# Performance work log

Measured on AMD Instinct MI355X. Metric: run time of the kernel, lower is better.

The kernel has to match this reference:

```python
import jax, jax.numpy as jnp
import numpy as np

E = 8      # number of experts (sublayers)
N = 8192   # tokens / batch rows
D = 1024   # sublayer input size (max_sublayer_input_size)
H = 2048   # sublayer output size
O = 1024   # output_encoding_size


def setup_inputs() -> dict:
    key = jax.random.key(0)
    k0, k1, k2, k3 = jax.random.split(key, 4)
    x_feat = jax.random.normal(k0, (N, D), dtype=jnp.float32)
    expert_idx = jax.random.randint(k1, (N,), 0, E)  # exclusive (top-1) routing
    # Stacked expert params: sublayers = Linear(D,H), encoders = Linear(H,O)
    W1 = jax.random.normal(k2, (E, D, H), dtype=jnp.float32) * (1.0 / np.sqrt(D))
    b1 = jnp.zeros((E, H), dtype=jnp.float32)
    W2 = jax.random.normal(k3, (E, H, O), dtype=jnp.float32) * (1.0 / np.sqrt(H))
    b2 = jnp.zeros((E, O), dtype=jnp.float32)
    return {"x_feat": x_feat, "W1": W1, "b1": b1, "W2": W2, "b2": b2,
            "expert_idx": expert_idx}


def reference(x_feat, W1, b1, W2, b2, expert_idx):
    # one-hot sublayer_mask (last E columns of the original x)
    onehot = jax.nn.one_hot(expert_idx, E, dtype=x_feat.dtype)  # [N, E]
    # Exclusive dispatch: each token goes through exactly one expert.
    # Structural loop over the fixed E experts; combine via the one-hot mask
    # (equivalent to the original gather -> sublayer -> encoder -> scatter).
    enc = jnp.zeros((x_feat.shape[0], O), dtype=x_feat.dtype)
    for i in range(E):
        h = x_feat @ W1[i] + b1[i]          # [N, H] sublayer
        y = h @ W2[i] + b2[i]               # [N, O] encoder
        enc = enc + onehot[:, i:i + 1] * y  # keep only rows routed to expert i
    # output = [encoded (O cols) | sublayer_mask (E cols)]
    return jnp.concatenate([enc, onehot], axis=1)
```

## Files before the change

kernel.cpp:

```cpp
#include <hip/hip_runtime.h>

#define NTOK 8192
#define DDIM 1024
#define HDIM 2048
#define ODIM 1024
#define NEXP 8
#define OUTW (ODIM + NEXP)

typedef __bf16 bf16_t;
typedef bf16_t bf16x8 __attribute__((ext_vector_type(8)));
typedef bf16_t bf16x4 __attribute__((ext_vector_type(4)));
typedef float f32x4 __attribute__((ext_vector_type(4)));

__device__ __forceinline__ void gld_lds16(bf16_t* lds, const bf16_t* g) {
  __builtin_amdgcn_global_load_lds(
      (__attribute__((address_space(1))) void*)g,
      (__attribute__((address_space(3))) void*)lds, 16, 0, 0);
}

__global__ void zero_cnt_kernel(int* cnt) {
  if (threadIdx.x < NEXP) cnt[threadIdx.x] = 0;
}

__global__ void route_kernel(const int* __restrict__ idx, float* __restrict__ out,
                             int* __restrict__ rank, int* cnt) {
  int n = blockIdx.x * 256 + threadIdx.x;
  int e = idx[n];
  rank[n] = atomicAdd(&cnt[e], 1);
  float* o = out + (size_t)n * OUTW + ODIM;
#pragma unroll
  for (int j = 0; j < NEXP; j++) o[j] = (j == e) ? 1.0f : 0.0f;
}

__global__ void scan_kernel(const int* __restrict__ cnt, int* __restrict__ off) {
  if (threadIdx.x == 0) {
    int s = 0;
    for (int e = 0; e < NEXP; e++) { off[e] = s; s += cnt[e]; }
  }
}

__global__ void gather_kernel(const float* __restrict__ x, const int* __restrict__ idx,
                              const int* __restrict__ rank, const int* __restrict__ off,
                              bf16_t* __restrict__ xg, int* __restrict__ tok_of_pos) {
  int n = blockIdx.x;
  int e = idx[n];
  int pos = off[e] + rank[n];
  if (threadIdx.x == 0) tok_of_pos[pos] = n;
  float4 v = ((const float4*)(x + (size_t)n * DDIM))[threadIdx.x];
  bf16x4 o;
  o[0] = (bf16_t)v.x; o[1] = (bf16_t)v.y; o[2] = (bf16_t)v.z; o[3] = (bf16_t)v.w;
  *(bf16x4*)(xg + (size_t)pos * DDIM + threadIdx.x * 4) = o;
}

__global__ void wtrans_kernel(const float* __restrict__ src, bf16_t* __restrict__ dst,
                              int R, int C) {
  __shared__ float t[64][65];
  int e = blockIdx.z;
  int c0 = blockIdx.x * 64, r0 = blockIdx.y * 64;
  int tx = threadIdx.x & 15, ty = threadIdx.x >> 4;
  const float* s = src + (size_t)e * R * C;
#pragma unroll
  for (int i = 0; i < 4; i++) {
    float4 v = *(const float4*)&s[(size_t)(r0 + ty + i * 16) * C + c0 + tx * 4];
    t[ty + i * 16][tx * 4 + 0] = v.x;
    t[ty + i * 16][tx * 4 + 1] = v.y;
    t[ty + i * 16][tx * 4 + 2] = v.z;
    t[ty + i * 16][tx * 4 + 3] = v.w;
  }
  __syncthreads();
  bf16_t* d = dst + (size_t)e * R * C;
#pragma unroll
  for (int i = 0; i < 4; i++) {
    bf16x4 o;
#pragma unroll
    for (int j = 0; j < 4; j++) o[j] = (bf16_t)t[tx * 4 + j][ty + i * 16];
    *(bf16x4*)&d[(size_t)(c0 + ty + i * 16) * R + r0 + tx * 4] = o;
  }
}

template <int KDIM, int NCOLS, bool TO_BF16>
__global__ __launch_bounds__(256) void gemm_kernel(
    const bf16_t* __restrict__ A, const bf16_t* __restrict__ Bt,
    const float* __restrict__ bias,
    const int* __restrict__ cnt, const int* __restrict__ off,
    const int* __restrict__ tok_of_pos,
    bf16_t* __restrict__ outb, float* __restrict__ outf) {
  const int e = blockIdx.z;
  const int mt = blockIdx.y;
  const int nt = blockIdx.x;
  const int count = cnt[e];
  if (mt * 128 >= count) return;
  const int base = off[e];

  __shared__ bf16_t lA[128 * 32];
  __shared__ bf16_t lB[128 * 32];

  const int tid = threadIdx.x;
  const int lane = tid & 63;
  const int wave = tid >> 6;
  const int mrow = lane & 15;
  const int q = lane >> 4;
  const int wm = (wave & 1) * 64;
  const int wn = (wave >> 1) * 64;

  const bf16_t* pA[2];
  const bf16_t* pB[2];
#pragma unroll
  for (int s = 0; s < 2; s++) {
    int lrow = wave * 32 + s * 16 + (lane >> 2);
    int gr = base + mt * 128 + lrow;
    if (gr > NTOK - 1) gr = NTOK - 1;
    pA[s] = A + (size_t)gr * KDIM + (lane & 3) * 8;
    int nrow = nt * 128 + lrow;
    pB[s] = Bt + ((size_t)e * NCOLS + nrow) * KDIM + (lane & 3) * 8;
  }

  f32x4 acc[4][4] = {};
  const bf16_t* la0 = &lA[(wm + mrow) * 32 + q * 8];
  const bf16_t* lb0 = &lB[(wn + mrow) * 32 + q * 8];

  for (int kk = 0; kk < KDIM; kk += 32) {
#pragma unroll
    for (int s = 0; s < 2; s++) {
      gld_lds16(&lA[(wave * 2 + s) * 512], pA[s] + kk);
      gld_lds16(&lB[(wave * 2 + s) * 512], pB[s] + kk);
    }
    __syncthreads();
    bf16x8 af[4], bfr[4];
#pragma unroll
    for (int i = 0; i < 4; i++) {
      af[i]  = *(const bf16x8*)(la0 + i * 16 * 32);
      bfr[i] = *(const bf16x8*)(lb0 + i * 16 * 32);
    }
#pragma unroll
    for (int i = 0; i < 4; i++)
#pragma unroll
      for (int j = 0; j < 4; j++)
        acc[i][j] = __builtin_amdgcn_mfma_f32_16x16x32_bf16(af[i], bfr[j], acc[i][j], 0, 0, 0);
    __syncthreads();
  }

  const int mlimit = count - mt * 128;
  float bs[4];
#pragma unroll
  for (int j = 0; j < 4; j++)
    bs[j] = bias[(size_t)e * NCOLS + nt * 128 + wn + j * 16 + mrow];

#pragma unroll
  for (int i = 0; i < 4; i++) {
#pragma unroll
    for (int r = 0; r < 4; r++) {
      int ml = wm + i * 16 + q * 4 + r;
      if (ml < mlimit) {
        int prow = base + mt * 128 + ml;
        if constexpr (TO_BF16) {
          bf16_t* orow = outb + (size_t)prow * NCOLS;
#pragma unroll
          for (int j = 0; j < 4; j++)
            orow[nt * 128 + wn + j * 16 + mrow] = (bf16_t)(acc[i][j][r] + bs[j]);
        } else {
          int tok = tok_of_pos[prow];
          float* orow = outf + (size_t)tok * OUTW;
#pragma unroll
          for (int j = 0; j < 4; j++)
            orow[nt * 128 + wn + j * 16 + mrow] = acc[i][j][r] + bs[j];
        }
      }
    }
  }
}

extern "C" void kernel_launch(void* const* d_in, const int* in_sizes, int n_in,
                              void* d_out, int out_size, void* d_ws, size_t ws_size,
                              hipStream_t stream) {
  const float* x  = (const float*)d_in[0];
  const float* W1 = (const float*)d_in[1];
  const float* b1 = (const float*)d_in[2];
  const float* W2 = (const float*)d_in[3];
  const float* b2 = (const float*)d_in[4];
  const int* idx  = (const int*)d_in[5];
  float* out = (float*)d_out;

  char* ws = (char*)d_ws;
  bf16_t* xg  = (bf16_t*)(ws);
  bf16_t* hg  = (bf16_t*)(ws + 16777216);
  bf16_t* Wt1 = (bf16_t*)(ws + 50331648);
  bf16_t* Wt2 = (bf16_t*)(ws + 83886080);
  int* tok    = (int*)(ws + 117440512);
  int* rank   = (int*)(ws + 117473280);
  int* cnt    = (int*)(ws + 117506048);
  int* off    = (int*)(ws + 117506080);

  zero_cnt_kernel<<<1, 64, 0, stream>>>(cnt);
  route_kernel<<<NTOK / 256, 256, 0, stream>>>(idx, out, rank, cnt);
  scan_kernel<<<1, 64, 0, stream>>>(cnt, off);
  gather_kernel<<<NTOK, 256, 0, stream>>>(x, idx, rank, off, xg, tok);
  wtrans_kernel<<<dim3(HDIM / 64, DDIM / 64, NEXP), 256, 0, stream>>>(W1, Wt1, DDIM, HDIM);
  wtrans_kernel<<<dim3(ODIM / 64, HDIM / 64, NEXP), 256, 0, stream>>>(W2, Wt2, HDIM, ODIM);
  gemm_kernel<DDIM, HDIM, true><<<dim3(HDIM / 128, NTOK / 128, NEXP), 256, 0, stream>>>(
      xg, Wt1, b1, cnt, off, tok, hg, nullptr);
  gemm_kernel<HDIM, ODIM, false><<<dim3(ODIM / 128, NTOK / 128, NEXP), 256, 0, stream>>>(
      hg, Wt2, b2, cnt, off, tok, nullptr, out);
}
```

Measured before the change: 356.3 us.

## Swizzle GEMM block order for L2 reuse and aggregate routing atomics per block

The GEMMs now run on a flattened 1D grid that is decoded so the expert index varies fastest, followed by a group of MTG M-tiles, then the N-tile. Consecutive workgroups therefore spread across experts and share weight and activation tiles, which is meant to improve L2/MALL locality and balance empty-tile early exits across CUs. The routing kernel also counts tokens per expert in shared memory and issues one global atomic per expert per block instead of one per token. Within-expert token order changes, but the result stays correct because ranks remain unique.

```diff
diff --git a/kernel.cpp b/kernel.cpp
--- a/kernel.cpp
+++ b/kernel.cpp
@@ -6,6 +6,7 @@
 #define ODIM 1024
 #define NEXP 8
 #define OUTW (ODIM + NEXP)
+#define MT_MAX 64
 
 typedef __bf16 bf16_t;
 typedef bf16_t bf16x8 __attribute__((ext_vector_type(8)));
@@ -24,9 +25,18 @@
 
 __global__ void route_kernel(const int* __restrict__ idx, float* __restrict__ out,
                              int* __restrict__ rank, int* cnt) {
-  int n = blockIdx.x * 256 + threadIdx.x;
+  __shared__ int lcnt[NEXP];
+  __shared__ int lbase[NEXP];
+  int t = threadIdx.x;
+  if (t < NEXP) lcnt[t] = 0;
+  __syncthreads();
+  int n = blockIdx.x * 256 + t;
   int e = idx[n];
-  rank[n] = atomicAdd(&cnt[e], 1);
+  int lr = atomicAdd(&lcnt[e], 1);
+  __syncthreads();
+  if (t < NEXP) lbase[t] = atomicAdd(&cnt[t], lcnt[t]);
+  __syncthreads();
+  rank[n] = lbase[e] + lr;
   float* o = out + (size_t)n * OUTW + ODIM;
 #pragma unroll
   for (int j = 0; j < NEXP; j++) o[j] = (j == e) ? 1.0f : 0.0f;
@@ -78,16 +88,23 @@
   }
 }
 
-template <int KDIM, int NCOLS, bool TO_BF16>
+template <int KDIM, int NCOLS, int MTG, bool TO_BF16>
 __global__ __launch_bounds__(256) void gemm_kernel(
     const bf16_t* __restrict__ A, const bf16_t* __restrict__ Bt,
     const float* __restrict__ bias,
     const int* __restrict__ cnt, const int* __restrict__ off,
     const int* __restrict__ tok_of_pos,
     bf16_t* __restrict__ outb, float* __restrict__ outf) {
-  const int e = blockIdx.z;
-  const int mt = blockIdx.y;
-  const int nt = blockIdx.x;
+  constexpr int NT = NCOLS / 128;
+  const int b = blockIdx.x;
+  const int e = b & 7;
+  int t = b >> 3;
+  const int mtl = t % MTG;
+  t /= MTG;
+  const int nt = t % NT;
+  const int g = t / NT;
+  const int mt = g * MTG + mtl;
+
   const int count = cnt[e];
   if (mt * 128 >= count) return;
   const int base = off[e];
@@ -197,8 +214,10 @@
   gather_kernel<<<NTOK, 256, 0, stream>>>(x, idx, rank, off, xg, tok);
   wtrans_kernel<<<dim3(HDIM / 64, DDIM / 64, NEXP), 256, 0, stream>>>(W1, Wt1, DDIM, HDIM);
   wtrans_kernel<<<dim3(ODIM / 64, HDIM / 64, NEXP), 256, 0, stream>>>(W2, Wt2, HDIM, ODIM);
-  gemm_kernel<DDIM, HDIM, true><<<dim3(HDIM / 128, NTOK / 128, NEXP), 256, 0, stream>>>(
+  gemm_kernel<DDIM, HDIM, 8, true>
+      <<<NEXP * MT_MAX * (HDIM / 128), 256, 0, stream>>>(
       xg, Wt1, b1, cnt, off, tok, hg, nullptr);
-  gemm_kernel<HDIM, ODIM, false><<<dim3(ODIM / 128, NTOK / 128, NEXP), 256, 0, stream>>>(
+  gemm_kernel<HDIM, ODIM, 4, false>
+      <<<NEXP * MT_MAX * (ODIM / 128), 256, 0, stream>>>(
       hg, Wt2, b2, cnt, off, tok, nullptr, out);
 }
```

New measurement: 314.6 us. -11.7%, faster.
